# Kernel tuning notes

Measured on AMD Instinct MI355X. Metric: run time of the kernel, lower is better.

The kernel has to match this reference:

```python
import jax, jax.numpy as jnp
import numpy as np

S, B, I, H, NH, HD, ML = 512, 32, 768, 256, 8, 32, 512
LN_EPS = 1e-5


def setup_inputs() -> dict:
    key = jax.random.key(0)
    ks = jax.random.split(key, 12)
    r = lambda k, shp, s=0.05: jax.random.normal(k, shp, dtype=jnp.float32) * s
    return {
        'x': r(ks[0], (S, B, I), 1.0),
        'Wi': r(ks[1], (5 * H, I)), 'bi': jnp.zeros((5 * H,), jnp.float32),
        'Wh': r(ks[2], (5 * H, H)), 'bh': jnp.zeros((5 * H,), jnp.float32),
        'Wt': r(ks[3], (H, 3 * H)), 'bt': jnp.zeros((H,), jnp.float32),
        'Wq': r(ks[4], (3, H, H)), 'bq': jnp.zeros((3, H), jnp.float32),
        'Wk': r(ks[5], (3, H, H)), 'bk': jnp.zeros((3, H), jnp.float32),
        'Wv': r(ks[6], (3, H, H)), 'bv': jnp.zeros((3, H), jnp.float32),
        'Wo': r(ks[7], (3, H, H)), 'bo': jnp.zeros((3, H), jnp.float32),
        'relpos': r(ks[8], (3, NH, ML, HD), 1.0),
        'ln_g': jnp.ones((H,), jnp.float32), 'ln_b': jnp.zeros((H,), jnp.float32),
    }


def cumsoftmax(z):
    return jnp.cumsum(jax.nn.softmax(z, axis=-1), axis=-1)


def _forward(x, Wi, bi, Wh, bh, Wt, bt, Wq, bq, Wk, bk, Wv, bv, Wo, bo, relpos, ln_g, ln_b):
    # --- sequential PFN (ON-LSTM style) recurrence over time ---
    def step(carry, xt):
        h, c_in = carry
        gates = xt @ Wi.T + bi + h @ Wh.T + bh            # [B, 5H]
        c, eg_cin, rg_cin, eg_c, rg_c = jnp.split(gates, 5, axis=-1)
        eg_cin = 1.0 - cumsoftmax(eg_cin)
        rg_cin = cumsoftmax(rg_cin)
        eg_c = 1.0 - cumsoftmax(eg_c)
        rg_c = cumsoftmax(rg_c)
        c = jnp.tanh(c)
        ov_c = rg_c * eg_c
        up_c = rg_c - ov_c
        dn_c = eg_c - ov_c
        ov_i = rg_cin * eg_cin
        up_i = rg_cin - ov_i
        dn_i = eg_cin - ov_i
        share = ov_i * c_in + ov_c * c
        c_re = up_i * c_in + up_c * c + share
        c_ner = dn_i * c_in + dn_c * c + share
        h_re = jnp.tanh(c_re)
        h_ner = jnp.tanh(c_ner)
        h_share = jnp.tanh(share)
        c_out = jnp.concatenate([c_re, c_ner, share], axis=-1) @ Wt.T + bt
        h_out = jnp.tanh(c_out)
        return (h_out, c_out), (h_ner, h_re, h_share)

    init = (jnp.zeros((B, H), x.dtype), jnp.zeros((B, H), x.dtype))
    _, (h_ner, h_re, h_share) = jax.lax.scan(step, init, x)   # each [S, B, H]

    # --- relative multi-head attention (no 1/sqrt(d) scaling, as in source) ---
    def attn(hb, i):
        b, s, d = hb.shape
        q = (hb @ Wq[i].T + bq[i]).reshape(b, s, NH, HD)
        k = (hb @ Wk[i].T + bk[i]).reshape(b, s, NH, HD)
        v = (hb @ Wv[i].T + bv[i]).reshape(b, s, NH, HD)
        scores = jnp.einsum('bqnd,bknd->bnqk', q, k) \
               + jnp.einsum('bqnd,nkd->bnqk', q, relpos[i][:, :s])
        w = jax.nn.softmax(scores, axis=-1)
        o = jnp.einsum('bnqk,bknd->bqnd', w, v).reshape(b, s, d)
        return o @ Wo[i].T + bo[i]

    def layer_norm(z):
        m = z.mean(-1, keepdims=True)
        v = z.var(-1, keepdims=True)
        return (z - m) / jnp.sqrt(v + LN_EPS) * ln_g + ln_b

    def apply_attention(h_sbd, i):
        hb = jnp.transpose(h_sbd, (1, 0, 2))      # [B, S, H]
        y = layer_norm(hb + attn(hb, i))          # residual + LN (dropout=0, eval)
        return jnp.transpose(y, (1, 0, 2))        # back to [S, B, H]

    out_ner = apply_attention(h_ner, 0)
    out_re = apply_attention(h_re, 1)
    out_share = apply_attention(h_re, 2)  # faithful to source: h_share attn consumes h_re
    return out_ner, out_re, out_share


def reference(x, Wi, bi, Wh, bh, Wt, bt, Wq, bq, Wk, bk, Wv, bv, Wo, bo, relpos, ln_g, ln_b):
    return _forward(x, Wi, bi, Wh, bh, Wt, bt, Wq, bq, Wk, bk, Wv, bv, Wo, bo, relpos, ln_g, ln_b)
```

## Files before the change

kernel.cpp:

```cpp
#include <hip/hip_runtime.h>
#include <hip/hip_bf16.h>

#define SDIM 512
#define BDIM 32

typedef _Float16 v2h __attribute__((ext_vector_type(2)));
typedef short bf16x8 __attribute__((ext_vector_type(8)));
typedef float f32x4 __attribute__((ext_vector_type(4)));

__device__ __forceinline__ float b2f(ushort u) {
    union { uint32_t i; float f; } v; v.i = ((uint32_t)u) << 16; return v.f;
}
__device__ __forceinline__ ushort f2b(float f) {
    union { float f; uint32_t i; } v; v.f = f;
    uint32_t u = v.i;
    return (ushort)((u + 0x7fffu + ((u >> 16) & 1u)) >> 16);
}
__device__ __forceinline__ ushort f2h(float f) {
    union { _Float16 h; ushort u; } v; v.h = (_Float16)f; return v.u;
}
__device__ __forceinline__ float dot2(uint32_t w, uint32_t h, float acc) {
#if __has_builtin(__builtin_amdgcn_fdot2)
    union { uint32_t u; v2h v; } a, b;
    a.u = w; b.u = h;
    return __builtin_amdgcn_fdot2(a.v, b.v, acc, false);
#else
    union { uint32_t u; v2h v; } a, b;
    a.u = w; b.u = h;
    return acc + (float)a.v.x * (float)b.v.x + (float)a.v.y * (float)b.v.y;
#endif
}
__device__ __forceinline__ float ftanh(float x) {
    const float t = __expf(2.f * x);
    return 1.f - 2.f * __builtin_amdgcn_rcpf(t + 1.f);
}

#define DCHUNK8C(WQ, HQ, ACC)                                                  \
    {                                                                          \
        uint4 wA = *(const uint4*)(WQ);                                        \
        uint4 wB = *(const uint4*)((WQ) + 4);                                  \
        uint4 hA = *(const uint4*)(HQ);                                        \
        uint4 hB = *(const uint4*)((HQ) + 4);                                  \
        ACC = dot2(wA.x, hA.x, ACC);                                           \
        ACC = dot2(wA.y, hA.y, ACC);                                           \
        ACC = dot2(wA.z, hA.z, ACC);                                           \
        ACC = dot2(wA.w, hA.w, ACC);                                           \
        ACC = dot2(wB.x, hB.x, ACC);                                           \
        ACC = dot2(wB.y, hB.y, ACC);                                           \
        ACC = dot2(wB.z, hB.z, ACC);                                           \
        ACC = dot2(wB.w, hB.w, ACC);                                           \
    }

__global__ __launch_bounds__(256) void transpose_kernel(
    const float* __restrict__ src, float* __restrict__ dst, int R, int C)
{
    __shared__ float t[32][33];
    const int bx = blockIdx.x * 32, by = blockIdx.y * 32;
    const int x = threadIdx.x & 31, y = threadIdx.x >> 5;
    #pragma unroll
    for (int dy = 0; dy < 32; dy += 8)
        t[y + dy][x] = src[(size_t)(by + y + dy) * C + bx + x];
    __syncthreads();
    #pragma unroll
    for (int dy = 0; dy < 32; dy += 8)
        dst[(size_t)(bx + y + dy) * R + by + x] = t[x][y + dy];
}

__global__ __launch_bounds__(256) void pack8_kernel(
    const float* __restrict__ in, uint32_t* __restrict__ out, int P, int J)
{
    const int idx = blockIdx.x * 256 + threadIdx.x;
    if (idx >= P * J) return;
    const int p = idx / J, j = idx - p * J;
    const ushort lo = f2h(in[(size_t)(2 * p) * J + j]);
    const ushort hi = f2h(in[(size_t)(2 * p + 1) * J + j]);
    out[(((size_t)(p >> 3) * J + j) << 3) + (p & 7)] = ((uint32_t)hi << 16) | lo;
}

__global__ __launch_bounds__(256) void cvt_bf16_kernel(
    const float* __restrict__ in, ushort* __restrict__ out, int n)
{
    const int stride = gridDim.x * 256;
    for (int i = blockIdx.x * 256 + threadIdx.x; i < n; i += stride)
        out[i] = f2b(in[i]);
}

__global__ __launch_bounds__(256) void addvec_kernel(
    const float* __restrict__ a, const float* __restrict__ b,
    float* __restrict__ o, int n)
{
    const int i = blockIdx.x * 256 + threadIdx.x;
    if (i < n) o[i] = a[i] + b[i];
}

__global__ __launch_bounds__(256) void mfma_gemm128_kernel(
    const ushort* __restrict__ A16, const ushort* __restrict__ B16,
    const float* __restrict__ bias, float* __restrict__ C, int N, int K)
{
    __shared__ ushort As[128][40];
    __shared__ ushort Bs[64][40];
    const int tid = threadIdx.x;
    const int tile_m = blockIdx.x * 128, tile_n = blockIdx.y * 64;
    const int r = tid >> 2, c = (tid & 3) * 8;
    const int am0 = tile_m + r, am1 = tile_m + 64 + r;
    const int bn = tile_n + r;
    const int w = tid >> 6, lane = tid & 63;
    const int mi = lane & 15, quad = lane >> 4;
    f32x4 acc[2][4] = {};

    for (int k0 = 0; k0 < K; k0 += 32) {
        *(uint4*)&As[r][c]      = *(const uint4*)(A16 + (size_t)am0 * K + k0 + c);
        *(uint4*)&As[64 + r][c] = *(const uint4*)(A16 + (size_t)am1 * K + k0 + c);
        *(uint4*)&Bs[r][c]      = *(const uint4*)(B16 + (size_t)bn * K + k0 + c);
        __syncthreads();
        const bf16x8 af0 = *(const bf16x8*)&As[w * 32 + mi][quad * 8];
        const bf16x8 af1 = *(const bf16x8*)&As[w * 32 + 16 + mi][quad * 8];
        #pragma unroll
        for (int j = 0; j < 4; j++) {
            const bf16x8 bf = *(const bf16x8*)&Bs[j * 16 + mi][quad * 8];
            acc[0][j] = __builtin_amdgcn_mfma_f32_16x16x32_bf16(af0, bf, acc[0][j], 0, 0, 0);
            acc[1][j] = __builtin_amdgcn_mfma_f32_16x16x32_bf16(af1, bf, acc[1][j], 0, 0, 0);
        }
        __syncthreads();
    }
    #pragma unroll
    for (int j = 0; j < 4; j++) {
        const int gn = tile_n + j * 16 + mi;
        const float bv = bias[gn];
        #pragma unroll
        for (int f = 0; f < 2; f++) {
            #pragma unroll
            for (int rr = 0; rr < 4; rr++) {
                const int gm = tile_m + w * 32 + f * 16 + quad * 4 + rr;
                C[(size_t)gm * N + gn] = acc[f][j][rr] + bv;
            }
        }
    }
}

__global__ __launch_bounds__(256) void qkv_gemm128_kernel(
    const ushort* __restrict__ A16,
    const ushort* __restrict__ Wq, const ushort* __restrict__ Wk,
    const ushort* __restrict__ Wv,
    const float* __restrict__ bq, const float* __restrict__ bk,
    const float* __restrict__ bv, const float* __restrict__ rp,
    float* __restrict__ qo, float* __restrict__ ko, float* __restrict__ vo)
{
    __shared__ ushort As[128][40];
    __shared__ ushort Bs[3][64][40];
    const int tid = threadIdx.x;
    const int tile_m = blockIdx.x * 128, tile_n = blockIdx.y * 64;
    const int r = tid >> 2, c = (tid & 3) * 8;
    const int am0 = tile_m + r, am1 = tile_m + 64 + r;
    const int ar0 = (am0 & (SDIM - 1)) * BDIM + (am0 >> 9);
    const int ar1 = (am1 & (SDIM - 1)) * BDIM + (am1 >> 9);
    const int bn = tile_n + r;
    const int w = tid >> 6, lane = tid & 63;
    const int mi = lane & 15, quad = lane >> 4;
    f32x4 acc[3][2][4] = {};

    for (int k0 = 0; k0 < 256; k0 += 32) {
        *(uint4*)&As[r][c]      = *(const uint4*)(A16 + (size_t)ar0 * 256 + k0 + c);
        *(uint4*)&As[64 + r][c] = *(const uint4*)(A16 + (size_t)ar1 * 256 + k0 + c);
        *(uint4*)&Bs[0][r][c]   = *(const uint4*)(Wq + (size_t)bn * 256 + k0 + c);
        *(uint4*)&Bs[1][r][c]   = *(const uint4*)(Wk + (size_t)bn * 256 + k0 + c);
        *(uint4*)&Bs[2][r][c]   = *(const uint4*)(Wv + (size_t)bn * 256 + k0 + c);
        __syncthreads();
        const bf16x8 af0 = *(const bf16x8*)&As[w * 32 + mi][quad * 8];
        const bf16x8 af1 = *(const bf16x8*)&As[w * 32 + 16 + mi][quad * 8];
        #pragma unroll
        for (int z = 0; z < 3; z++) {
            #pragma unroll
            for (int j = 0; j < 4; j++) {
                const bf16x8 bf = *(const bf16x8*)&Bs[z][j * 16 + mi][quad * 8];
                acc[z][0][j] = __builtin_amdgcn_mfma_f32_16x16x32_bf16(af0, bf, acc[z][0][j], 0, 0, 0);
                acc[z][1][j] = __builtin_amdgcn_mfma_f32_16x16x32_bf16(af1, bf, acc[z][1][j], 0, 0, 0);
            }
        }
        __syncthreads();
    }
    #pragma unroll
    for (int z = 0; z < 3; z++) {
        const float* bias = (z == 0) ? bq : (z == 1) ? bk : bv;
        float* out = (z == 0) ? qo : (z == 1) ? ko : vo;
        #pragma unroll
        for (int j = 0; j < 4; j++) {
            const int gn = tile_n + j * 16 + mi;
            const float bb = bias[gn];
            #pragma unroll
            for (int f = 0; f < 2; f++) {
                #pragma unroll
                for (int rr = 0; rr < 4; rr++) {
                    const int gm = tile_m + w * 32 + f * 16 + quad * 4 + rr;
                    float v = acc[z][f][j][rr] + bb;
                    if (z == 1) {
                        const int sgm = gm & (SDIM - 1);
                        v += rp[((gn >> 5) << 14) + (sgm << 5) + (gn & 31)];
                    }
                    out[(size_t)gm * 256 + gn] = v;
                }
            }
        }
    }
}

__global__ __launch_bounds__(1024) void scan_kernel(
    const float* __restrict__ gx,
    const uint32_t* __restrict__ Wh8,
    const uint32_t* __restrict__ Wt8,
    const float* __restrict__ bt,
    ushort* __restrict__ h_ner,
    ushort* __restrict__ h_re)
{
    const int b = blockIdx.x;
    const int tid = threadIdx.x;
    __shared__ float cs[256], g[1280], ext[1024];
    __shared__ alignas(16) uint32_t hs_pk[128];
    __shared__ alignas(16) uint32_t cat_pk[384];
    __shared__ float rsum[16];
    if (tid < 256) cs[tid] = 0.f;
    if (tid < 128) hs_pk[tid] = 0u;
    __syncthreads();
    const int lane = tid & 63;
    const int ch = tid >> 8;
    const int wch = (tid >> 6) & 3;
    const int er = tid & 255;
    const int ep = tid >> 8;
    const uint32_t* wmain = Wh8 + (size_t)tid * 8;
    const uint32_t* wext  = Wh8 + ((size_t)(ep * 4) * 1280 + 1024 + er) * 8;
    const uint32_t* wtp   = Wt8 + ((size_t)(ep * 12) * 256 + er) * 8;

    for (int t = 0; t < SDIM; t++) {
        const float* gxr = gx + (size_t)(t * BDIM + b) * 1280;
        {
            float a0 = 0.f, a1 = 0.f;
            #pragma unroll 2
            for (int q8 = 0; q8 < 16; q8 += 2) {
                DCHUNK8C(wmain + (size_t)q8 * (1280 * 8), hs_pk + q8 * 8, a0);
                DCHUNK8C(wmain + (size_t)(q8 + 1) * (1280 * 8), hs_pk + q8 * 8 + 8, a1);
            }
            g[tid] = gxr[tid] + a0 + a1;
        }
        {
            float ae = (ep == 0) ? gxr[1024 + er] : 0.f;
            #pragma unroll
            for (int i = 0; i < 4; i++)
                DCHUNK8C(wext + (size_t)i * (1280 * 8), hs_pk + (ep * 4 + i) * 8, ae);
            ext[ep * 256 + er] = ae;
        }
        __syncthreads();
        if (tid < 256) g[tid] = ftanh(g[tid]);
        float v;
        if (tid >= 768) {
            const int r_ = tid - 768;
            v = ext[r_] + ext[256 + r_] + ext[512 + r_] + ext[768 + r_];
        } else {
            v = g[256 + tid];
        }
        const float e = __expf(v);
        float wsum = e;
        #pragma unroll
        for (int off = 32; off >= 1; off >>= 1) wsum += __shfl_xor(wsum, off, 64);
        if (lane == 0) rsum[ch * 4 + wch] = wsum;
        float cum = e;
        #pragma unroll
        for (int off = 1; off <= 32; off <<= 1) {
            float tsh = __shfl_up(cum, (unsigned)off, 64);
            if (lane >= off) cum += tsh;
        }
        __syncthreads();
        const float tot = rsum[ch * 4] + rsum[ch * 4 + 1] + rsum[ch * 4 + 2] + rsum[ch * 4 + 3];
        float prev = 0.f;
        if (wch > 0) prev += rsum[ch * 4];
        if (wch > 1) prev += rsum[ch * 4 + 1];
        if (wch > 2) prev += rsum[ch * 4 + 2];
        float r = (cum + prev) * __builtin_amdgcn_rcpf(tot);
        if (ch == 0 || ch == 2) r = 1.f - r;
        g[256 + tid] = r;
        __syncthreads();
        if (tid < 256) {
            const float c = g[tid];
            const float egi = g[256 + tid], rgi = g[512 + tid];
            const float egc = g[768 + tid], rgc = g[1024 + tid];
            const float cin = cs[tid];
            const float ovc = rgc * egc, upc = rgc - ovc, dnc = egc - ovc;
            const float ovi = rgi * egi, upi = rgi - ovi, dni = egi - ovi;
            const float share = ovi * cin + ovc * c;
            const float cre = upi * cin + upc * c + share;
            const float cner = dni * cin + dnc * c + share;
            ((_Float16*)cat_pk)[tid]       = (_Float16)cre;
            ((_Float16*)cat_pk)[256 + tid] = (_Float16)cner;
            ((_Float16*)cat_pk)[512 + tid] = (_Float16)share;
            const size_t ob = (size_t)(t * BDIM + b) * 256 + tid;
            h_re[ob] = f2b(ftanh(cre));
            h_ner[ob] = f2b(ftanh(cner));
        }
        __syncthreads();
        {
            float s0 = 0.f, s1 = 0.f;
            #pragma unroll 2
            for (int i = 0; i < 12; i += 2) {
                DCHUNK8C(wtp + (size_t)i * (256 * 8), cat_pk + (ep * 12 + i) * 8, s0);
                DCHUNK8C(wtp + (size_t)(i + 1) * (256 * 8), cat_pk + (ep * 12 + i + 1) * 8, s1);
            }
            g[ep * 256 + er] = s0 + s1;
        }
        __syncthreads();
        if (tid < 256) {
            const float co = g[tid] + g[256 + tid] + g[512 + tid] + g[768 + tid] + bt[tid];
            cs[tid] = co;
            ((_Float16*)hs_pk)[tid] = (_Float16)ftanh(co);
        }
        __syncthreads();
    }
}

__global__ __launch_bounds__(512) void attn_kernel(
    const float* __restrict__ q_ws, const float* __restrict__ kk_ws,
    const float* __restrict__ v_ws, ushort* __restrict__ o16)
{
    __shared__ float sc[8 * 516];
    __shared__ float ps[8 * 256];
    __shared__ float sinv[8];
    const int bn = blockIdx.x;
    const int b = bn >> 3, n = bn & 7;
    const int tid = threadIdx.x;
    const int w = tid >> 6, lane = tid & 63;
    const int ki = w * 64 + lane;
    float kv[32];
    {
        const float4* kp = (const float4*)(kk_ws + (size_t)(b * 512 + ki) * 256 + n * 32);
        #pragma unroll
        for (int d4 = 0; d4 < 8; d4++) {
            float4 x = kp[d4];
            kv[4 * d4] = x.x; kv[4 * d4 + 1] = x.y; kv[4 * d4 + 2] = x.z; kv[4 * d4 + 3] = x.w;
        }
    }
    const int rr = lane >> 3, dq = lane & 7;

    for (int q0 = 0; q0 < 512; q0 += 8) {
        const float* qbase = q_ws + (size_t)(b * 512 + q0) * 256 + n * 32;
        #pragma unroll 1
        for (int r = 0; r < 8; r++) {
            const float4* q4 = (const float4*)(qbase + r * 256);
            float s0 = 0.f, s1 = 0.f;
            #pragma unroll
            for (int d4 = 0; d4 < 8; d4 += 2) {
                const float4 qa = q4[d4];
                const float4 qb = q4[d4 + 1];
                s0 += qa.x * kv[4 * d4] + qa.y * kv[4 * d4 + 1]
                    + qa.z * kv[4 * d4 + 2] + qa.w * kv[4 * d4 + 3];
                s1 += qb.x * kv[4 * d4 + 4] + qb.y * kv[4 * d4 + 5]
                    + qb.z * kv[4 * d4 + 6] + qb.w * kv[4 * d4 + 7];
            }
            sc[r * 516 + ki] = s0 + s1;
        }
        __syncthreads();
        {
            float* row = sc + w * 516;
            float4 a = ((const float4*)row)[lane];
            float4 c4 = ((const float4*)row)[lane + 64];
            float mx = fmaxf(fmaxf(fmaxf(a.x, a.y), fmaxf(a.z, a.w)),
                             fmaxf(fmaxf(c4.x, c4.y), fmaxf(c4.z, c4.w)));
            #pragma unroll
            for (int off = 32; off >= 1; off >>= 1) mx = fmaxf(mx, __shfl_xor(mx, off, 64));
            a.x = __expf(a.x - mx); a.y = __expf(a.y - mx);
            a.z = __expf(a.z - mx); a.w = __expf(a.w - mx);
            c4.x = __expf(c4.x - mx); c4.y = __expf(c4.y - mx);
            c4.z = __expf(c4.z - mx); c4.w = __expf(c4.w - mx);
            float sm = a.x + a.y + a.z + a.w + c4.x + c4.y + c4.z + c4.w;
            #pragma unroll
            for (int off = 32; off >= 1; off >>= 1) sm += __shfl_xor(sm, off, 64);
            ((float4*)row)[lane] = a;
            ((float4*)row)[lane + 64] = c4;
            if (lane == 0) sinv[w] = 1.f / sm;
        }
        __syncthreads();
        {
            float4 acc0 = {0.f, 0.f, 0.f, 0.f};
            float4 acc1 = {0.f, 0.f, 0.f, 0.f};
            const float* erow = sc + rr * 516 + w * 64;
            const float* vbase = v_ws + (size_t)(b * 512 + w * 64) * 256 + n * 32 + dq * 4;
            #pragma unroll 4
            for (int j = 0; j < 64; j += 2) {
                const float e0 = erow[j], e1 = erow[j + 1];
                float4 v0 = *(const float4*)(vbase + (size_t)j * 256);
                float4 v1 = *(const float4*)(vbase + (size_t)(j + 1) * 256);
                acc0.x += e0 * v0.x; acc0.y += e0 * v0.y;
                acc0.z += e0 * v0.z; acc0.w += e0 * v0.w;
                acc1.x += e1 * v1.x; acc1.y += e1 * v1.y;
                acc1.z += e1 * v1.z; acc1.w += e1 * v1.w;
            }
            float4 acc = {acc0.x + acc1.x, acc0.y + acc1.y,
                          acc0.z + acc1.z, acc0.w + acc1.w};
            ((float4*)ps)[tid] = acc;
        }
        __syncthreads();
        if (tid < 256) {
            const int r2 = tid >> 5, d = tid & 31;
            float s = 0.f;
            #pragma unroll
            for (int ww = 0; ww < 8; ww++) s += ps[ww * 256 + r2 * 32 + d];
            o16[(size_t)(b * 512 + q0 + r2) * 256 + n * 32 + d] = f2b(s * sinv[r2]);
        }
        __syncthreads();
    }
}

__global__ __launch_bounds__(256) void ln_kernel(
    const float* __restrict__ proj, const ushort* __restrict__ hsrc,
    const float* __restrict__ lng, const float* __restrict__ lnb,
    float* __restrict__ outp)
{
    const int m = blockIdx.x;
    const int j = threadIdx.x;
    const int b = m >> 9, s = m & 511;
    const size_t oidx = (size_t)(s * 32 + b) * 256 + j;
    const float y = proj[(size_t)m * 256 + j] + b2f(hsrc[oidx]);
    float sum = y, sq = y * y;
    #pragma unroll
    for (int off = 32; off >= 1; off >>= 1) {
        sum += __shfl_xor(sum, off, 64);
        sq += __shfl_xor(sq, off, 64);
    }
    __shared__ float r1[4], r2[4];
    const int wv = j >> 6;
    if ((j & 63) == 0) { r1[wv] = sum; r2[wv] = sq; }
    __syncthreads();
    const float ts = r1[0] + r1[1] + r1[2] + r1[3];
    const float tq = r2[0] + r2[1] + r2[2] + r2[3];
    const float mean = ts * (1.f / 256.f);
    const float var = tq * (1.f / 256.f) - mean * mean;
    const float o = (y - mean) * rsqrtf(var + 1e-5f) * lng[j] + lnb[j];
    outp[oidx] = o;
}

extern "C" void kernel_launch(void* const* d_in, const int* in_sizes, int n_in,
                              void* d_out, int out_size, void* d_ws, size_t ws_size,
                              hipStream_t stream) {
    (void)in_sizes; (void)n_in; (void)out_size; (void)ws_size;
    const float* x   = (const float*)d_in[0];
    const float* Wi  = (const float*)d_in[1];
    const float* bi  = (const float*)d_in[2];
    const float* Wh  = (const float*)d_in[3];
    const float* bh  = (const float*)d_in[4];
    const float* Wt  = (const float*)d_in[5];
    const float* bt  = (const float*)d_in[6];
    const float* Wq  = (const float*)d_in[7];
    const float* bq  = (const float*)d_in[8];
    const float* Wk  = (const float*)d_in[9];
    const float* bk  = (const float*)d_in[10];
    const float* Wv  = (const float*)d_in[11];
    const float* bv  = (const float*)d_in[12];
    const float* Wo  = (const float*)d_in[13];
    const float* bo  = (const float*)d_in[14];
    const float* rp  = (const float*)d_in[15];
    const float* lng = (const float*)d_in[16];
    const float* lnb = (const float*)d_in[17];
    float* outp = (float*)d_out;

    float* ws = (float*)d_ws;
    float* gx    = ws;
    float* q_ws  = ws;
    float* kk_ws = ws + 4194304;
    float* v_ws  = ws + 8388608;
    float* pj_ws = ws + 12582912;
    ushort* o16  = (ushort*)(ws + 16777216);
    ushort* hner16 = (ushort*)(ws + 20971520);
    ushort* hre16  = (ushort*)(ws + 23068672);
    uint32_t* Wh8 = (uint32_t*)(ws + 25165824);
    uint32_t* Wt8 = (uint32_t*)(ws + 25329664);
    ushort* Wq16 = (ushort*)(ws + 25427968);
    ushort* Wk16 = (ushort*)(ws + 25526272);
    ushort* Wv16 = (ushort*)(ws + 25624576);
    ushort* Wo16 = (ushort*)(ws + 25722880);

    ushort* x16  = (ushort*)outp;
    ushort* Wi16 = (ushort*)(outp + 6291456);
    float* WhT   = outp + 6782976;
    float* WtT   = outp + 7110656;
    float* bsum  = outp + 7307264;

    transpose_kernel<<<dim3(8, 40), 256, 0, stream>>>(Wh, WhT, 1280, 256);
    transpose_kernel<<<dim3(24, 8), 256, 0, stream>>>(Wt, WtT, 256, 768);
    pack8_kernel<<<dim3(640), 256, 0, stream>>>(WhT, Wh8, 128, 1280);
    pack8_kernel<<<dim3(384), 256, 0, stream>>>(WtT, Wt8, 384, 256);
    addvec_kernel<<<dim3(5), 256, 0, stream>>>(bi, bh, bsum, 1280);
    cvt_bf16_kernel<<<dim3(4096), 256, 0, stream>>>(x, x16, 12582912);
    cvt_bf16_kernel<<<dim3(1024), 256, 0, stream>>>(Wi, Wi16, 983040);
    cvt_bf16_kernel<<<dim3(256), 256, 0, stream>>>(Wq, Wq16, 196608);
    cvt_bf16_kernel<<<dim3(256), 256, 0, stream>>>(Wk, Wk16, 196608);
    cvt_bf16_kernel<<<dim3(256), 256, 0, stream>>>(Wv, Wv16, 196608);
    cvt_bf16_kernel<<<dim3(256), 256, 0, stream>>>(Wo, Wo16, 196608);

    mfma_gemm128_kernel<<<dim3(128, 20), 256, 0, stream>>>(
        x16, Wi16, bsum, gx, 1280, 768);

    scan_kernel<<<dim3(32), dim3(1024), 0, stream>>>(gx, Wh8, Wt8, bt, hner16, hre16);

    for (int i = 0; i < 3; i++) {
        const ushort* src16 = (i == 0) ? hner16 : hre16;
        qkv_gemm128_kernel<<<dim3(128, 4), 256, 0, stream>>>(
            src16, Wq16 + (size_t)i * 65536, Wk16 + (size_t)i * 65536,
            Wv16 + (size_t)i * 65536, bq + i * 256, bk + i * 256, bv + i * 256,
            rp + (size_t)i * 131072, q_ws, kk_ws, v_ws);
        attn_kernel<<<dim3(256), dim3(512), 0, stream>>>(q_ws, kk_ws, v_ws, o16);
        mfma_gemm128_kernel<<<dim3(128, 4), 256, 0, stream>>>(
            o16, Wo16 + (size_t)i * 65536, bo + i * 256, pj_ws, 256, 256);
        ln_kernel<<<dim3(16384), dim3(256), 0, stream>>>(
            pj_ws, src16, lng, lnb, outp + (size_t)i * 4194304);
    }
}
```

Before: 5.916 ms.

## Fuse weight prep kernels, deepen GEMM K tiles, add scan accumulators

```diff
diff --git a/kernel.cpp b/kernel.cpp
--- a/kernel.cpp
+++ b/kernel.cpp
@@ -51,38 +51,39 @@
         ACC = dot2(wB.w, hB.w, ACC);                                           \
     }
 
-__global__ __launch_bounds__(256) void transpose_kernel(
-    const float* __restrict__ src, float* __restrict__ dst, int R, int C)
-{
-    __shared__ float t[32][33];
-    const int bx = blockIdx.x * 32, by = blockIdx.y * 32;
-    const int x = threadIdx.x & 31, y = threadIdx.x >> 5;
-    #pragma unroll
-    for (int dy = 0; dy < 32; dy += 8)
-        t[y + dy][x] = src[(size_t)(by + y + dy) * C + bx + x];
-    __syncthreads();
-    #pragma unroll
-    for (int dy = 0; dy < 32; dy += 8)
-        dst[(size_t)(bx + y + dy) * R + by + x] = t[x][y + dy];
-}
-
-__global__ __launch_bounds__(256) void pack8_kernel(
-    const float* __restrict__ in, uint32_t* __restrict__ out, int P, int J)
+__global__ __launch_bounds__(256) void pack8d_kernel(
+    const float* __restrict__ src, int ld, uint32_t* __restrict__ out, int P, int J)
 {
     const int idx = blockIdx.x * 256 + threadIdx.x;
     if (idx >= P * J) return;
-    const int p = idx / J, j = idx - p * J;
-    const ushort lo = f2h(in[(size_t)(2 * p) * J + j]);
-    const ushort hi = f2h(in[(size_t)(2 * p + 1) * J + j]);
+    const int j = idx / P, p = idx - j * P;
+    const ushort lo = f2h(src[(size_t)j * ld + 2 * p]);
+    const ushort hi = f2h(src[(size_t)j * ld + 2 * p + 1]);
     out[(((size_t)(p >> 3) * J + j) << 3) + (p & 7)] = ((uint32_t)hi << 16) | lo;
 }
 
-__global__ __launch_bounds__(256) void cvt_bf16_kernel(
-    const float* __restrict__ in, ushort* __restrict__ out, int n)
+__global__ __launch_bounds__(256) void cvt_bf16x2_kernel(
+    const float* __restrict__ a, ushort* __restrict__ oa, int na,
+    const float* __restrict__ b, ushort* __restrict__ ob, int nb)
 {
     const int stride = gridDim.x * 256;
-    for (int i = blockIdx.x * 256 + threadIdx.x; i < n; i += stride)
-        out[i] = f2b(in[i]);
+    for (int i = blockIdx.x * 256 + threadIdx.x; i < na + nb; i += stride) {
+        if (i < na) oa[i] = f2b(a[i]);
+        else ob[i - na] = f2b(b[i - na]);
+    }
+}
+__global__ __launch_bounds__(256) void cvt_bf16x4_kernel(
+    const float* __restrict__ a, const float* __restrict__ b,
+    const float* __restrict__ c, const float* __restrict__ d,
+    ushort* __restrict__ oa, ushort* __restrict__ ob,
+    ushort* __restrict__ oc, ushort* __restrict__ od, int n)
+{
+    const int i = blockIdx.x * 256 + threadIdx.x;
+    if (i >= 4 * n) return;
+    const int which = i / n, j = i - which * n;
+    const float* s = which == 0 ? a : which == 1 ? b : which == 2 ? c : d;
+    ushort* o = which == 0 ? oa : which == 1 ? ob : which == 2 ? oc : od;
+    o[j] = f2b(s[j]);
 }
 
 __global__ __launch_bounds__(256) void addvec_kernel(
@@ -97,29 +98,36 @@
     const ushort* __restrict__ A16, const ushort* __restrict__ B16,
     const float* __restrict__ bias, float* __restrict__ C, int N, int K)
 {
-    __shared__ ushort As[128][40];
-    __shared__ ushort Bs[64][40];
+    __shared__ ushort As[128][72];
+    __shared__ ushort Bs[64][72];
     const int tid = threadIdx.x;
     const int tile_m = blockIdx.x * 128, tile_n = blockIdx.y * 64;
-    const int r = tid >> 2, c = (tid & 3) * 8;
-    const int am0 = tile_m + r, am1 = tile_m + 64 + r;
-    const int bn = tile_n + r;
+    const int ra = tid >> 1, ca = (tid & 1) * 32;
+    const int rb = tid >> 2, cb = (tid & 3) * 16;
     const int w = tid >> 6, lane = tid & 63;
     const int mi = lane & 15, quad = lane >> 4;
     f32x4 acc[2][4] = {};
 
-    for (int k0 = 0; k0 < K; k0 += 32) {
-        *(uint4*)&As[r][c]      = *(const uint4*)(A16 + (size_t)am0 * K + k0 + c);
-        *(uint4*)&As[64 + r][c] = *(const uint4*)(A16 + (size_t)am1 * K + k0 + c);
-        *(uint4*)&Bs[r][c]      = *(const uint4*)(B16 + (size_t)bn * K + k0 + c);
-        __syncthreads();
-        const bf16x8 af0 = *(const bf16x8*)&As[w * 32 + mi][quad * 8];
-        const bf16x8 af1 = *(const bf16x8*)&As[w * 32 + 16 + mi][quad * 8];
-        #pragma unroll
-        for (int j = 0; j < 4; j++) {
-            const bf16x8 bf = *(const bf16x8*)&Bs[j * 16 + mi][quad * 8];
-            acc[0][j] = __builtin_amdgcn_mfma_f32_16x16x32_bf16(af0, bf, acc[0][j], 0, 0, 0);
-            acc[1][j] = __builtin_amdgcn_mfma_f32_16x16x32_bf16(af1, bf, acc[1][j], 0, 0, 0);
+    for (int k0 = 0; k0 < K; k0 += 64) {
+        const uint4* ap = (const uint4*)(A16 + (size_t)(tile_m + ra) * K + k0 + ca);
+        *(uint4*)&As[ra][ca]      = ap[0];
+        *(uint4*)&As[ra][ca + 8]  = ap[1];
+        *(uint4*)&As[ra][ca + 16] = ap[2];
+        *(uint4*)&As[ra][ca + 24] = ap[3];
+        const uint4* bp = (const uint4*)(B16 + (size_t)(tile_n + rb) * K + k0 + cb);
+        *(uint4*)&Bs[rb][cb]     = bp[0];
+        *(uint4*)&Bs[rb][cb + 8] = bp[1];
+        __syncthreads();
+        #pragma unroll
+        for (int kk = 0; kk < 64; kk += 32) {
+            const bf16x8 af0 = *(const bf16x8*)&As[w * 32 + mi][quad * 8 + kk];
+            const bf16x8 af1 = *(const bf16x8*)&As[w * 32 + 16 + mi][quad * 8 + kk];
+            #pragma unroll
+            for (int j = 0; j < 4; j++) {
+                const bf16x8 bf = *(const bf16x8*)&Bs[j * 16 + mi][quad * 8 + kk];
+                acc[0][j] = __builtin_amdgcn_mfma_f32_16x16x32_bf16(af0, bf, acc[0][j], 0, 0, 0);
+                acc[1][j] = __builtin_amdgcn_mfma_f32_16x16x32_bf16(af1, bf, acc[1][j], 0, 0, 0);
+            }
         }
         __syncthreads();
     }
@@ -146,35 +154,47 @@
     const float* __restrict__ bv, const float* __restrict__ rp,
     float* __restrict__ qo, float* __restrict__ ko, float* __restrict__ vo)
 {
-    __shared__ ushort As[128][40];
-    __shared__ ushort Bs[3][64][40];
+    __shared__ ushort As[128][72];
+    __shared__ ushort Bs[3][64][72];
     const int tid = threadIdx.x;
     const int tile_m = blockIdx.x * 128, tile_n = blockIdx.y * 64;
-    const int r = tid >> 2, c = (tid & 3) * 8;
-    const int am0 = tile_m + r, am1 = tile_m + 64 + r;
-    const int ar0 = (am0 & (SDIM - 1)) * BDIM + (am0 >> 9);
-    const int ar1 = (am1 & (SDIM - 1)) * BDIM + (am1 >> 9);
-    const int bn = tile_n + r;
+    const int ra = tid >> 1, ca = (tid & 1) * 32;
+    const int am = tile_m + ra;
+    const int ar = (am & (SDIM - 1)) * BDIM + (am >> 9);
+    const int rb = tid >> 2, cb = (tid & 3) * 16;
+    const int bn = tile_n + rb;
     const int w = tid >> 6, lane = tid & 63;
     const int mi = lane & 15, quad = lane >> 4;
     f32x4 acc[3][2][4] = {};
 
-    for (int k0 = 0; k0 < 256; k0 += 32) {
-        *(uint4*)&As[r][c]      = *(const uint4*)(A16 + (size_t)ar0 * 256 + k0 + c);
-        *(uint4*)&As[64 + r][c] = *(const uint4*)(A16 + (size_t)ar1 * 256 + k0 + c);
-        *(uint4*)&Bs[0][r][c]   = *(const uint4*)(Wq + (size_t)bn * 256 + k0 + c);
-        *(uint4*)&Bs[1][r][c]   = *(const uint4*)(Wk + (size_t)bn * 256 + k0 + c);
-        *(uint4*)&Bs[2][r][c]   = *(const uint4*)(Wv + (size_t)bn * 256 + k0 + c);
-        __syncthreads();
-        const bf16x8 af0 = *(const bf16x8*)&As[w * 32 + mi][quad * 8];
-        const bf16x8 af1 = *(const bf16x8*)&As[w * 32 + 16 + mi][quad * 8];
-        #pragma unroll
-        for (int z = 0; z < 3; z++) {
-            #pragma unroll
-            for (int j = 0; j < 4; j++) {
-                const bf16x8 bf = *(const bf16x8*)&Bs[z][j * 16 + mi][quad * 8];
-                acc[z][0][j] = __builtin_amdgcn_mfma_f32_16x16x32_bf16(af0, bf, acc[z][0][j], 0, 0, 0);
-                acc[z][1][j] = __builtin_amdgcn_mfma_f32_16x16x32_bf16(af1, bf, acc[z][1][j], 0, 0, 0);
+    for (int k0 = 0; k0 < 256; k0 += 64) {
+        const uint4* ap = (const uint4*)(A16 + (size_t)ar * 256 + k0 + ca);
+        *(uint4*)&As[ra][ca]      = ap[0];
+        *(uint4*)&As[ra][ca + 8]  = ap[1];
+        *(uint4*)&As[ra][ca + 16] = ap[2];
+        *(uint4*)&As[ra][ca + 24] = ap[3];
+        const uint4* qp = (const uint4*)(Wq + (size_t)bn * 256 + k0 + cb);
+        *(uint4*)&Bs[0][rb][cb]     = qp[0];
+        *(uint4*)&Bs[0][rb][cb + 8] = qp[1];
+        const uint4* kp = (const uint4*)(Wk + (size_t)bn * 256 + k0 + cb);
+        *(uint4*)&Bs[1][rb][cb]     = kp[0];
+        *(uint4*)&Bs[1][rb][cb + 8] = kp[1];
+        const uint4* vp = (const uint4*)(Wv + (size_t)bn * 256 + k0 + cb);
+        *(uint4*)&Bs[2][rb][cb]     = vp[0];
+        *(uint4*)&Bs[2][rb][cb + 8] = vp[1];
+        __syncthreads();
+        #pragma unroll
+        for (int kk = 0; kk < 64; kk += 32) {
+            const bf16x8 af0 = *(const bf16x8*)&As[w * 32 + mi][quad * 8 + kk];
+            const bf16x8 af1 = *(const bf16x8*)&As[w * 32 + 16 + mi][quad * 8 + kk];
+            #pragma unroll
+            for (int z = 0; z < 3; z++) {
+                #pragma unroll
+                for (int j = 0; j < 4; j++) {
+                    const bf16x8 bf = *(const bf16x8*)&Bs[z][j * 16 + mi][quad * 8 + kk];
+                    acc[z][0][j] = __builtin_amdgcn_mfma_f32_16x16x32_bf16(af0, bf, acc[z][0][j], 0, 0, 0);
+                    acc[z][1][j] = __builtin_amdgcn_mfma_f32_16x16x32_bf16(af1, bf, acc[z][1][j], 0, 0, 0);
+                }
             }
         }
         __syncthreads();
@@ -232,21 +252,25 @@
 
     for (int t = 0; t < SDIM; t++) {
         const float* gxr = gx + (size_t)(t * BDIM + b) * 1280;
+        const float gxv = gxr[tid];
         {
-            float a0 = 0.f, a1 = 0.f;
-            #pragma unroll 2
-            for (int q8 = 0; q8 < 16; q8 += 2) {
-                DCHUNK8C(wmain + (size_t)q8 * (1280 * 8), hs_pk + q8 * 8, a0);
-                DCHUNK8C(wmain + (size_t)(q8 + 1) * (1280 * 8), hs_pk + q8 * 8 + 8, a1);
-            }
-            g[tid] = gxr[tid] + a0 + a1;
+            float a0 = 0.f, a1 = 0.f, a2 = 0.f, a3 = 0.f;
+            #pragma unroll
+            for (int q8 = 0; q8 < 16; q8 += 4) {
+                DCHUNK8C(wmain + (size_t)q8 * 10240, hs_pk + q8 * 8, a0);
+                DCHUNK8C(wmain + (size_t)(q8 + 1) * 10240, hs_pk + q8 * 8 + 8, a1);
+                DCHUNK8C(wmain + (size_t)(q8 + 2) * 10240, hs_pk + q8 * 8 + 16, a2);
+                DCHUNK8C(wmain + (size_t)(q8 + 3) * 10240, hs_pk + q8 * 8 + 24, a3);
+            }
+            g[tid] = gxv + (a0 + a1) + (a2 + a3);
         }
         {
-            float ae = (ep == 0) ? gxr[1024 + er] : 0.f;
-            #pragma unroll
-            for (int i = 0; i < 4; i++)
-                DCHUNK8C(wext + (size_t)i * (1280 * 8), hs_pk + (ep * 4 + i) * 8, ae);
-            ext[ep * 256 + er] = ae;
+            float e0 = (ep == 0) ? gxr[1024 + er] : 0.f, e1 = 0.f;
+            DCHUNK8C(wext + (size_t)0 * 10240, hs_pk + (ep * 4) * 8, e0);
+            DCHUNK8C(wext + (size_t)1 * 10240, hs_pk + (ep * 4 + 1) * 8, e1);
+            DCHUNK8C(wext + (size_t)2 * 10240, hs_pk + (ep * 4 + 2) * 8, e0);
+            DCHUNK8C(wext + (size_t)3 * 10240, hs_pk + (ep * 4 + 3) * 8, e1);
+            ext[ep * 256 + er] = e0 + e1;
         }
         __syncthreads();
         if (tid < 256) g[tid] = ftanh(g[tid]);
@@ -297,13 +321,15 @@
         }
         __syncthreads();
         {
-            float s0 = 0.f, s1 = 0.f;
-            #pragma unroll 2
-            for (int i = 0; i < 12; i += 2) {
-                DCHUNK8C(wtp + (size_t)i * (256 * 8), cat_pk + (ep * 12 + i) * 8, s0);
-                DCHUNK8C(wtp + (size_t)(i + 1) * (256 * 8), cat_pk + (ep * 12 + i + 1) * 8, s1);
-            }
-            g[ep * 256 + er] = s0 + s1;
+            float s0 = 0.f, s1 = 0.f, s2 = 0.f, s3 = 0.f;
+            #pragma unroll
+            for (int i = 0; i < 12; i += 4) {
+                DCHUNK8C(wtp + (size_t)i * 2048, cat_pk + (ep * 12 + i) * 8, s0);
+                DCHUNK8C(wtp + (size_t)(i + 1) * 2048, cat_pk + (ep * 12 + i + 1) * 8, s1);
+                DCHUNK8C(wtp + (size_t)(i + 2) * 2048, cat_pk + (ep * 12 + i + 2) * 8, s2);
+                DCHUNK8C(wtp + (size_t)(i + 3) * 2048, cat_pk + (ep * 12 + i + 3) * 8, s3);
+            }
+            g[ep * 256 + er] = (s0 + s1) + (s2 + s3);
         }
         __syncthreads();
         if (tid < 256) {
@@ -477,21 +503,14 @@
 
     ushort* x16  = (ushort*)outp;
     ushort* Wi16 = (ushort*)(outp + 6291456);
-    float* WhT   = outp + 6782976;
-    float* WtT   = outp + 7110656;
     float* bsum  = outp + 7307264;
 
-    transpose_kernel<<<dim3(8, 40), 256, 0, stream>>>(Wh, WhT, 1280, 256);
-    transpose_kernel<<<dim3(24, 8), 256, 0, stream>>>(Wt, WtT, 256, 768);
-    pack8_kernel<<<dim3(640), 256, 0, stream>>>(WhT, Wh8, 128, 1280);
-    pack8_kernel<<<dim3(384), 256, 0, stream>>>(WtT, Wt8, 384, 256);
+    pack8d_kernel<<<dim3(640), 256, 0, stream>>>(Wh, 256, Wh8, 128, 1280);
+    pack8d_kernel<<<dim3(384), 256, 0, stream>>>(Wt, 768, Wt8, 384, 256);
     addvec_kernel<<<dim3(5), 256, 0, stream>>>(bi, bh, bsum, 1280);
-    cvt_bf16_kernel<<<dim3(4096), 256, 0, stream>>>(x, x16, 12582912);
-    cvt_bf16_kernel<<<dim3(1024), 256, 0, stream>>>(Wi, Wi16, 983040);
-    cvt_bf16_kernel<<<dim3(256), 256, 0, stream>>>(Wq, Wq16, 196608);
-    cvt_bf16_kernel<<<dim3(256), 256, 0, stream>>>(Wk, Wk16, 196608);
-    cvt_bf16_kernel<<<dim3(256), 256, 0, stream>>>(Wv, Wv16, 196608);
-    cvt_bf16_kernel<<<dim3(256), 256, 0, stream>>>(Wo, Wo16, 196608);
+    cvt_bf16x2_kernel<<<dim3(4096), 256, 0, stream>>>(x, x16, 12582912, Wi, Wi16, 983040);
+    cvt_bf16x4_kernel<<<dim3(3072), 256, 0, stream>>>(
+        Wq, Wk, Wv, Wo, Wq16, Wk16, Wv16, Wo16, 196608);
 
     mfma_gemm128_kernel<<<dim3(128, 20), 256, 0, stream>>>(
         x16, Wi16, bsum, gx, 1280, 768);
```

Result: slower. 12.45 ms (+110.4%).
